# Optimization experiments

Hardware: AMD Instinct MI355X
Metric: run time of the kernel (lower is better)

Reference implementation:

```python
import jax, jax.numpy as jnp
import numpy as np

TWO_PI = np.float32(2.0 * np.pi)


def setup_inputs() -> dict:
    H, W = 2048, 2048
    MAX_COC = 21  # gain_params['max_CoC']
    key = jax.random.key(0)
    k1, k2 = jax.random.split(key)
    image = jax.random.uniform(k1, (H, W, 3), dtype=jnp.float32)
    # per-pixel circle-of-confusion kernel size (what GetSparseTensor derives from the depth map)
    kernel_size_flatten = jax.random.randint(k2, (H * W,), 0, MAX_COC + 1, dtype=jnp.int32)
    return {"image": image, "kernel_size_flatten": kernel_size_flatten, "max_coc": MAX_COC}


def reference(image, kernel_size_flatten, max_coc):
    """Spatially-variant Gaussian defocus blur.

    Faithful to CudaGetDefocusWeightsKernel: each input pixel px with
    kernel_size k > 1 scatters image[px] * N(offset; sigma=k/6) to all
    in-bounds neighbors within k//2; pixels with k <= 1 pass through
    (weight 1.0 at themselves). Out-of-bounds targets are skipped (the
    kernel clamps the loop range), realized here by a discarded padding
    ring on the output buffer.
    """
    H, W, C = image.shape
    half_max = max_coc // 2  # static Python int

    ks = kernel_size_flatten.reshape(H, W)            # [H, W] int
    half_k = (ks // 2).astype(jnp.float32)            # kernel_size // 2
    blur = ks > 1                                     # [H, W] bool
    sigma = ks.astype(jnp.float32) / 6.0
    sigma_safe = jnp.where(blur, sigma, 1.0)          # avoid 0-div on identity pixels
    inv_2s2 = 0.5 / (sigma_safe * sigma_safe)         # [H, W]
    norm = 1.0 / (TWO_PI * sigma_safe * sigma_safe)   # [H, W]

    offs = jnp.arange(-half_max, half_max + 1)
    dys, dxs = jnp.meshgrid(offs, offs, indexing="ij")
    dys, dxs = dys.reshape(-1), dxs.reshape(-1)       # [K^2] scatter offsets

    pad = half_max
    out0 = jnp.zeros((H + 2 * pad, W + 2 * pad, C), image.dtype)

    def step(out, off):
        dy, dx = off
        d2 = (dy * dy + dx * dx).astype(jnp.float32)
        in_win = (jnp.abs(dy).astype(jnp.float32) <= half_k) & (
            jnp.abs(dx).astype(jnp.float32) <= half_k
        )
        gw = jnp.exp(-d2 * inv_2s2) * norm            # [H, W] Gaussian weight
        wmap = jnp.where(blur & in_win, gw, 0.0)
        wmap = jnp.where((~blur) & (dy == 0) & (dx == 0), 1.0, wmap)
        contrib = image * wmap[..., None]             # [H, W, C]
        y0, x0 = pad + dy, pad + dx
        cur = jax.lax.dynamic_slice(out, (y0, x0, 0), (H, W, C))
        out = jax.lax.dynamic_update_slice(out, cur + contrib, (y0, x0, 0))
        return out, None

    out, _ = jax.lax.scan(step, out0, (dys, dxs))
    return out[pad:pad + H, pad:pad + W, :]
```

## Files before the change

### kernel.cpp

```cpp
#include <hip/hip_runtime.h>
#include <hip/hip_fp16.h>

#define IMG_W 2048
#define IMG_H 2048
#define HALF  10
#define TILE_H 32
#define TILE_W 64
#define LH (TILE_H + 2*HALF)
#define LW (TILE_W + 2*HALF)
#define NSTG (LH * LW)

#define L_KSD 51
#define L_KSB 204
#define L_NDW (22 * L_KSD)

__device__ __forceinline__ __half2 h2(uint u)  { union { uint a; __half2 b; } c; c.a = u; return c.b; }
__device__ __forceinline__ uint pack2(float a, float b) {
    return (uint)__half_as_ushort(__float2half(a)) |
           ((uint)__half_as_ushort(__float2half(b)) << 16);
}
__device__ __forceinline__ float wyv(int k, int oy) {
    int a = abs(oy), hk = k >> 1;
    if (a > hk) return 0.f;
    if (k <= 1) return 1.f;
    float kk = (float)(k * k);
    return expf(-(float)(oy * oy) * 18.f / kk) * 5.7295780f / kk;
}
__device__ __forceinline__ float wxv(int k, int ox) {
    int a = abs(ox), hk = k >> 1;
    if (a > hk) return 0.f;
    if (k <= 1) return 1.f;
    float kk = (float)(k * k);
    return expf(-(float)(ox * ox) * 18.f / kk);
}

#define FMA_LO(acc, px, w) \
    asm("v_pk_fma_f16 %0, %1, %2, %0 op_sel:[0,0,0] op_sel_hi:[0,1,1]" \
        : "+v"(acc) : "v"(px), "v"(w))
#define FMA_HI(acc, px, w) \
    asm("v_pk_fma_f16 %0, %1, %2, %0 op_sel:[1,0,0] op_sel_hi:[1,1,1]" \
        : "+v"(acc) : "v"(px), "v"(w))
#define MUL_WYLO(d, wx2, wy2) \
    asm("v_pk_mul_f16 %0, %1, %2 op_sel:[0,0] op_sel_hi:[1,0]" \
        : "=v"(d) : "v"(wx2), "v"(wy2))
#define MUL_WYHI(d, wx2, wy2) \
    asm("v_pk_mul_f16 %0, %1, %2 op_sel:[0,1] op_sel_hi:[1,1]" \
        : "=v"(d) : "v"(wx2), "v"(wy2))

__global__ __launch_bounds__(256)
void defocus_asm_kernel(const float* __restrict__ img,
                        const int* __restrict__ ks,
                        float* __restrict__ out)
{
    __shared__ uint  lutw[L_NDW + 2];
    __shared__ uint2 tile[NSTG];

    const int tid = threadIdx.x;
    const int X0 = blockIdx.x * TILE_W;
    const int Y0 = blockIdx.y * TILE_H;

    for (int i = tid; i < L_NDW; i += 256) {
        int k = i / L_KSD;
        int d = i - k * L_KSD;
        float lo = 0.f, hi = 0.f;
        if (d < 22) {
            lo = wyv(k, d - 10);
            hi = wyv(k, d - 11);
        } else if (d < 36) {
            int j = d - 22;
            lo = wxv(k, 2 * j - 13);
            hi = wxv(k, 2 * j - 12);
        } else if (d < 50) {
            int j = d - 36;
            lo = wxv(k, 2 * j - 12);
            hi = wxv(k, 2 * j - 11);
        }
        lutw[i] = pack2(lo, hi);
    }

    for (int i = tid; i < NSTG; i += 256) {
        int r = i / LW;
        int c = i - r * LW;
        int gy = Y0 - HALF + r;
        int gx = X0 - HALF + c;
        float fr = 0.f, fg = 0.f, fb = 0.f;
        uint koffB = 0;
        if (gy >= 0 && gy < IMG_H && gx >= 0 && gx < IMG_W) {
            int p = gy * IMG_W + gx;
            fr = img[p * 3 + 0];
            fg = img[p * 3 + 1];
            fb = img[p * 3 + 2];
            koffB = (uint)(ks[p] * L_KSB);
        }
        uint2 v;
        v.x = pack2(fr, fg);
        v.y = koffB | ((uint)__half_as_ushort(__float2half(fb)) << 16);
        tile[r * LW + (c & 3) * 21 + (c >> 2)] = v;
    }
    __syncthreads();

    const int tx = tid & 15;
    const int ty = tid >> 4;
    const int colbase = tx * 4;
    const int rowbase = ty * 2;
    const int pxbase  = rowbase * LW + tx;

    uint A32[2][3] = {{0,0,0},{0,0,0}}, A10[2][3] = {{0,0,0},{0,0,0}};
    float mc[2][4][3];
    #pragma unroll
    for (int r = 0; r < 2; ++r)
        #pragma unroll
        for (int c = 0; c < 3; ++c)
            mc[r][0][c] = mc[r][1][c] = mc[r][2][c] = mc[r][3][c] = 0.f;

#define ROW(aa)                                                                    \
    { _Pragma("unroll")                                                            \
      for (int b = 0; b < 24; ++b) {                                               \
          uint2 p = tile[pxbase + (aa) * LW + (b & 3) * 21 + (b >> 2)];            \
          const char* wp = (const char*)lutw + (p.y & 0xffffu);                    \
          uint wy2 = *(const uint*)(wp + 4 * (aa));                                \
          uint w32, w10;    \
          if ((b & 1) == 0) {                                                      \
              w32 = *(const uint*)(wp + 4 * (22 + (b >> 1)));                      \
              w10 = *(const uint*)(wp + 4 * (23 + (b >> 1)));                      \
          } else {                                                                 \
              w32 = *(const uint*)(wp + 4 * (36 + ((b - 1) >> 1)));                \
              w10 = *(const uint*)(wp + 4 * (36 + ((b + 1) >> 1)));                \
          }                                                                        \
          uint W320, W100, W321, W101;                                             \
          MUL_WYLO(W320, w32, wy2);                                                \
          MUL_WYLO(W100, w10, wy2);                                                \
          MUL_WYHI(W321, w32, wy2);                                                \
          MUL_WYHI(W101, w10, wy2);                                                \
          FMA_LO(A32[0][0], p.x, W320);                                            \
          FMA_HI(A32[0][1], p.x, W320);                                            \
          FMA_HI(A32[0][2], p.y, W320);                                            \
          FMA_LO(A10[0][0], p.x, W100);                                            \
          FMA_HI(A10[0][1], p.x, W100);                                            \
          FMA_HI(A10[0][2], p.y, W100);                                            \
          FMA_LO(A32[1][0], p.x, W321);                                            \
          FMA_HI(A32[1][1], p.x, W321);                                            \
          FMA_HI(A32[1][2], p.y, W321);                                            \
          FMA_LO(A10[1][0], p.x, W101);                                            \
          FMA_HI(A10[1][1], p.x, W101);                                            \
          FMA_HI(A10[1][2], p.y, W101);                                            \
      } }

#define FLUSH()                                                        \
    { _Pragma("unroll")                                                \
      for (int r = 0; r < 2; ++r) {                                    \
          _Pragma("unroll")                                            \
          for (int c = 0; c < 3; ++c) {                                \
              float2 f3 = __half22float2(h2(A32[r][c]));               \
              float2 f1 = __half22float2(h2(A10[r][c]));               \
              mc[r][3][c] += f3.x; mc[r][2][c] += f3.y;                \
              mc[r][1][c] += f1.x; mc[r][0][c] += f1.y;                \
              A32[r][c] = 0; A10[r][c] = 0;                            \
          }                                                            \
      } }

    #pragma unroll 1
    for (int ap = 0; ap < 11; ++ap) {
        ROW(2 * ap);
        ROW(2 * ap + 1);
        FLUSH();
    }

    #pragma unroll
    for (int r = 0; r < 2; ++r) {
        int gy = Y0 + rowbase + r;
        #pragma unroll
        for (int m = 0; m < 4; ++m) {
            int gx = X0 + colbase + m;
            int o = (gy * IMG_W + gx) * 3;
            out[o + 0] = mc[r][m][0];
            out[o + 1] = mc[r][m][1];
            out[o + 2] = mc[r][m][2];
        }
    }
#undef ROW
#undef FLUSH
}

extern "C" void kernel_launch(void* const* d_in, const int* in_sizes, int n_in,
                              void* d_out, int out_size, void* d_ws, size_t ws_size,
                              hipStream_t stream) {
    const float* img = (const float*)d_in[0];
    const int*   ks  = (const int*)d_in[1];
    float* out = (float*)d_out;

    dim3 grid(IMG_W / TILE_W, IMG_H / TILE_H);
    dim3 block(256);
    defocus_asm_kernel<<<grid, block, 0, stream>>>(img, ks, out);
}
```

Before: 189.7 us.

## Compute 4x4 output pixels per thread with 64x64 tiles and paired row weights

Each thread now produces a 4x4 block of outputs instead of 4x2, and each block covers a 64x64 tile. The row-weight table is re-laid out so one 64-bit LDS load returns the vertical weights for four output rows, and each loaded source pixel and its horizontal weights feed twice as many FMAs. This cuts the per-output LDS traffic and halo re-staging cost. In exchange it uses more registers and shared memory, which can lower occupancy, and the launch bound asks for two blocks per CU.

```diff
diff --git a/kernel.cpp b/kernel.cpp
--- a/kernel.cpp
+++ b/kernel.cpp
@@ -4,14 +4,12 @@
 #define IMG_W 2048
 #define IMG_H 2048
 #define HALF  10
-#define TILE_H 32
-#define TILE_W 64
-#define LH (TILE_H + 2*HALF)
-#define LW (TILE_W + 2*HALF)
-#define NSTG (LH * LW)
+#define TILE  64
+#define LW 84
+#define NSTG (LW * LW)
 
-#define L_KSD 51
-#define L_KSB 204
+#define L_KSD 78
+#define L_KSB 312
 #define L_NDW (22 * L_KSD)
 
 __device__ __forceinline__ __half2 h2(uint u)  { union { uint a; __half2 b; } c; c.a = u; return c.b; }
@@ -47,31 +45,32 @@
     asm("v_pk_mul_f16 %0, %1, %2 op_sel:[0,1] op_sel_hi:[1,1]" \
         : "=v"(d) : "v"(wx2), "v"(wy2))
 
-__global__ __launch_bounds__(256)
-void defocus_asm_kernel(const float* __restrict__ img,
+__global__ __launch_bounds__(256, 2)
+void defocus_4x4_kernel(const float* __restrict__ img,
                         const int* __restrict__ ks,
                         float* __restrict__ out)
 {
-    __shared__ uint  lutw[L_NDW + 2];
-    __shared__ uint2 tile[NSTG];
+    __shared__ __align__(16) uint  lutw[L_NDW];
+    __shared__ __align__(16) uint2 tile[NSTG];
 
     const int tid = threadIdx.x;
-    const int X0 = blockIdx.x * TILE_W;
-    const int Y0 = blockIdx.y * TILE_H;
+    const int X0 = blockIdx.x * TILE;
+    const int Y0 = blockIdx.y * TILE;
 
     for (int i = tid; i < L_NDW; i += 256) {
         int k = i / L_KSD;
         int d = i - k * L_KSD;
         float lo = 0.f, hi = 0.f;
-        if (d < 22) {
-            lo = wyv(k, d - 10);
-            hi = wyv(k, d - 11);
-        } else if (d < 36) {
-            int j = d - 22;
-            lo = wxv(k, 2 * j - 13);
-            hi = wxv(k, 2 * j - 12);
-        } else if (d < 50) {
-            int j = d - 36;
+        if (d < 48) {
+            int aa = d >> 1, q = d & 1;
+            lo = wyv(k, aa - 10 - 2 * q);
+            hi = wyv(k, aa - 11 - 2 * q);
+        } else if (d < 62) {
+            int hh = d - 48;
+            lo = wxv(k, 2 * hh - 13);
+            hi = wxv(k, 2 * hh - 12);
+        } else if (d < 76) {
+            int j = d - 62;
             lo = wxv(k, 2 * j - 12);
             hi = wxv(k, 2 * j - 11);
         }
@@ -102,53 +101,52 @@
     const int tx = tid & 15;
     const int ty = tid >> 4;
     const int colbase = tx * 4;
-    const int rowbase = ty * 2;
+    const int rowbase = ty * 4;
     const int pxbase  = rowbase * LW + tx;
 
-    uint A32[2][3] = {{0,0,0},{0,0,0}}, A10[2][3] = {{0,0,0},{0,0,0}};
-    float mc[2][4][3];
+    uint A32[4][3] = {}, A10[4][3] = {};
+    float mc[4][4][3];
     #pragma unroll
-    for (int r = 0; r < 2; ++r)
+    for (int r = 0; r < 4; ++r)
         #pragma unroll
         for (int c = 0; c < 3; ++c)
             mc[r][0][c] = mc[r][1][c] = mc[r][2][c] = mc[r][3][c] = 0.f;
 
 #define ROW(aa)                                                                    \
-    { _Pragma("unroll")                                                            \
+    { const int pxrow = pxbase + (aa) * LW;                                        \
+      _Pragma("unroll")                                                            \
       for (int b = 0; b < 24; ++b) {                                               \
-          uint2 p = tile[pxbase + (aa) * LW + (b & 3) * 21 + (b >> 2)];            \
+          uint2 p = tile[pxrow + (b & 3) * 21 + (b >> 2)];                         \
           const char* wp = (const char*)lutw + (p.y & 0xffffu);                    \
-          uint wy2 = *(const uint*)(wp + 4 * (aa));                                \
-          uint w32, w10;    \
+          uint2 wy = *(const uint2*)(wp + 8 * (aa));                               \
+          const uint* wpu = (const uint*)wp;                                       \
+          uint w32, w10;   \
           if ((b & 1) == 0) {                                                      \
-              w32 = *(const uint*)(wp + 4 * (22 + (b >> 1)));                      \
-              w10 = *(const uint*)(wp + 4 * (23 + (b >> 1)));                      \
+              w32 = wpu[48 + (b >> 1)];                                            \
+              w10 = wpu[49 + (b >> 1)];                                            \
           } else {                                                                 \
-              w32 = *(const uint*)(wp + 4 * (36 + ((b - 1) >> 1)));                \
-              w10 = *(const uint*)(wp + 4 * (36 + ((b + 1) >> 1)));                \
+              w32 = wpu[62 + ((b - 1) >> 1)];                                      \
+              w10 = wpu[63 + ((b - 1) >> 1)];                                      \
           }                                                                        \
-          uint W320, W100, W321, W101;                                             \
-          MUL_WYLO(W320, w32, wy2);                                                \
-          MUL_WYLO(W100, w10, wy2);                                                \
-          MUL_WYHI(W321, w32, wy2);                                                \
-          MUL_WYHI(W101, w10, wy2);                                                \
-          FMA_LO(A32[0][0], p.x, W320);                                            \
-          FMA_HI(A32[0][1], p.x, W320);                                            \
-          FMA_HI(A32[0][2], p.y, W320);                                            \
-          FMA_LO(A10[0][0], p.x, W100);                                            \
-          FMA_HI(A10[0][1], p.x, W100);                                            \
-          FMA_HI(A10[0][2], p.y, W100);                                            \
-          FMA_LO(A32[1][0], p.x, W321);                                            \
-          FMA_HI(A32[1][1], p.x, W321);                                            \
-          FMA_HI(A32[1][2], p.y, W321);                                            \
-          FMA_LO(A10[1][0], p.x, W101);                                            \
-          FMA_HI(A10[1][1], p.x, W101);                                            \
-          FMA_HI(A10[1][2], p.y, W101);                                            \
+          uint W32[4], W10[4];                                                     \
+          MUL_WYLO(W32[0], w32, wy.x); MUL_WYHI(W32[1], w32, wy.x);                \
+          MUL_WYLO(W32[2], w32, wy.y); MUL_WYHI(W32[3], w32, wy.y);                \
+          MUL_WYLO(W10[0], w10, wy.x); MUL_WYHI(W10[1], w10, wy.x);                \
+          MUL_WYLO(W10[2], w10, wy.y); MUL_WYHI(W10[3], w10, wy.y);                \
+          _Pragma("unroll")                                                        \
+          for (int r = 0; r < 4; ++r) {                                            \
+              FMA_LO(A32[r][0], p.x, W32[r]);                                      \
+              FMA_HI(A32[r][1], p.x, W32[r]);                                      \
+              FMA_HI(A32[r][2], p.y, W32[r]);                                      \
+              FMA_LO(A10[r][0], p.x, W10[r]);                                      \
+              FMA_HI(A10[r][1], p.x, W10[r]);                                      \
+              FMA_HI(A10[r][2], p.y, W10[r]);                                      \
+          }                                                                        \
       } }
 
 #define FLUSH()                                                        \
     { _Pragma("unroll")                                                \
-      for (int r = 0; r < 2; ++r) {                                    \
+      for (int r = 0; r < 4; ++r) {                                    \
           _Pragma("unroll")                                            \
           for (int c = 0; c < 3; ++c) {                                \
               float2 f3 = __half22float2(h2(A32[r][c]));               \
@@ -160,14 +158,14 @@
       } }
 
     #pragma unroll 1
-    for (int ap = 0; ap < 11; ++ap) {
+    for (int ap = 0; ap < 12; ++ap) {
         ROW(2 * ap);
         ROW(2 * ap + 1);
         FLUSH();
     }
 
     #pragma unroll
-    for (int r = 0; r < 2; ++r) {
+    for (int r = 0; r < 4; ++r) {
         int gy = Y0 + rowbase + r;
         #pragma unroll
         for (int m = 0; m < 4; ++m) {
@@ -189,7 +187,7 @@
     const int*   ks  = (const int*)d_in[1];
     float* out = (float*)d_out;
 
-    dim3 grid(IMG_W / TILE_W, IMG_H / TILE_H);
+    dim3 grid(IMG_W / TILE, IMG_H / TILE);
     dim3 block(256);
-    defocus_asm_kernel<<<grid, block, 0, stream>>>(img, ks, out);
+    defocus_4x4_kernel<<<grid, block, 0, stream>>>(img, ks, out);
 }
```

Measured after the change: 218.7 us. 1.15x slower.
